# Optimization experiments

Measured on AMD Instinct MI355X. Metric: run time of the kernel, lower is better.

## Reference

```python
import jax, jax.numpy as jnp
import numpy as np


def gcn_conv(x, edge_index, W, b):
    """PyG GCNConv: linear transform, add self-loops, symmetric D^-1/2 A D^-1/2 aggregation, bias."""
    n = x.shape[0]
    h = x @ W  # [N, out] - transform before propagate (small out dim)
    loop = jnp.arange(n, dtype=edge_index.dtype)
    src = jnp.concatenate([edge_index[0], loop])
    dst = jnp.concatenate([edge_index[1], loop])
    deg = jax.ops.segment_sum(jnp.ones_like(dst, dtype=h.dtype), dst, num_segments=n)
    dinv = jnp.where(deg > 0, jax.lax.rsqrt(deg), 0.0)
    norm = dinv[src] * dinv[dst]  # [E+N]
    out = jax.ops.segment_sum(h[src] * norm[:, None], dst, num_segments=n)
    return out + b


def setup_inputs() -> dict:
    key = jax.random.key(0)
    k1, k2, k3, k4, k5, k6 = jax.random.split(key, 6)
    N, F_in, H, C, E = 100000, 128, 16, 2, 3200000
    x = jax.random.normal(k1, (N, F_in), dtype=jnp.float32)
    edge_index = jax.random.randint(k2, (2, E), 0, N, dtype=jnp.int32)
    # Glorot-style init for GCNConv weights
    W1 = jax.random.normal(k3, (F_in, H), dtype=jnp.float32) * (1.0 / np.sqrt(F_in))
    b1 = jnp.zeros((H,), dtype=jnp.float32)
    W2 = jax.random.normal(k4, (H, C), dtype=jnp.float32) * (1.0 / np.sqrt(H))
    b2 = jnp.zeros((C,), dtype=jnp.float32)
    return {"x": x, "edge_index": edge_index, "W1": W1, "b1": b1, "W2": W2, "b2": b2}


def reference(x, edge_index, W1, b1, W2, b2):
    h = gcn_conv(x, edge_index, W1, b1)
    h = jax.nn.relu(h)
    # F.dropout(training=self.training): eval mode -> identity (deterministic reference)
    h = gcn_conv(h, edge_index, W2, b2)
    return jax.nn.log_softmax(h, axis=1)
```

## Files before the change

kernel.cpp:

```cpp
#include <hip/hip_runtime.h>
#include <hip/hip_bf16.h>
#include <math.h>


#define F_IN 128
#define H1 16
#define C_OUT 2
#define SBS 1024
#define LOG_SBS 10
#define NSB_MAX 128
#define SRC_MASK 0x3FFFFF
#define CH1 4096
#define SLICE 128
#define NSLICE (SBS / SLICE)
#define PCAP 5632

typedef int ix4 __attribute__((ext_vector_type(4)));

__device__ __forceinline__ float bflo(unsigned u) { return __uint_as_float(u << 16); }
__device__ __forceinline__ float bfhi(unsigned u) { return __uint_as_float(u & 0xFFFF0000u); }

__global__ __launch_bounds__(256) void k_cnt_gemm1(
    const int* __restrict__ dst0, int* __restrict__ cntm,
    const float* __restrict__ x, const float* __restrict__ W1,
    __hip_bfloat16* __restrict__ h1b,
    int E, int NSB, int nblk, int N) {
    __shared__ int sc[NSB_MAX];
    __shared__ float w[F_IN * H1];
    __shared__ float xt[16 * F_IN];
    int t = threadIdx.x;
    if (blockIdx.x < (unsigned)nblk) {
        if (t < NSB_MAX) sc[t] = 0;
        __syncthreads();
        int e0 = blockIdx.x * CH1, e1 = min(e0 + CH1, E);
        int n4 = (e1 - e0) >> 2;
        const ix4* d4 = (const ix4*)(dst0 + e0);
        for (int i = t; i < n4; i += 256) {
            ix4 d = __builtin_nontemporal_load(&d4[i]);
            atomicAdd(&sc[((unsigned)d.x) >> LOG_SBS], 1);
            atomicAdd(&sc[((unsigned)d.y) >> LOG_SBS], 1);
            atomicAdd(&sc[((unsigned)d.z) >> LOG_SBS], 1);
            atomicAdd(&sc[((unsigned)d.w) >> LOG_SBS], 1);
        }
        for (int e = e0 + n4 * 4 + t; e < e1; e += 256)
            atomicAdd(&sc[((unsigned)dst0[e]) >> LOG_SBS], 1);
        __syncthreads();
        for (int b = t; b < NSB; b += 256)
            cntm[(size_t)b * nblk + blockIdx.x] = sc[b];
    } else {
        int node0 = (blockIdx.x - nblk) * 16;
        const float4* W14 = (const float4*)W1;
        float4* w4 = (float4*)w;
        for (int i = t; i < F_IN * H1 / 4; i += 256) w4[i] = W14[i];
        const float4* x4 = (const float4*)x;
        float4* xt4 = (float4*)xt;
        for (int i = t; i < 16 * F_IN / 4; i += 256) {
            int r = i >> 5;
            int node = node0 + r;
            xt4[i] = (node < N) ? x4[(size_t)node * 32 + (i & 31)]
                                : make_float4(0.f, 0.f, 0.f, 0.f);
        }
        __syncthreads();
        int nsub = t >> 4, f = t & 15;
        int node = node0 + nsub;
        if (node < N) {
            const float* xr = xt + nsub * F_IN;
            float acc = 0.0f;
            #pragma unroll 16
            for (int k = 0; k < F_IN; ++k)
                acc = fmaf(xr[k], w[k * H1 + f], acc);
            h1b[(size_t)node * H1 + f] = __float2bfloat16(acc);
        }
    }
}

__global__ __launch_bounds__(1024) void k_cscan(
    int* __restrict__ cntm, int* __restrict__ tot, int* __restrict__ rp,
    int NSB, int nblk, int E) {
    __shared__ int s[1024];
    int b = blockIdx.x, t = threadIdx.x;
    int* row = cntm + (size_t)b * nblk;
    int own = (t < nblk) ? row[t] : 0;
    s[t] = own;
    __syncthreads();
    for (int off = 1; off < 1024; off <<= 1) {
        int v = (t >= off) ? s[t - off] : 0;
        __syncthreads();
        s[t] += v;
        __syncthreads();
    }
    if (t < nblk) row[t] = s[t] - own;
    if (t == 0) tot[b] = s[1023];
    if (b == 0 && t == 0) rp[NSB * SBS] = E;
}

__global__ __launch_bounds__(256) void k_scat1(
    const int* __restrict__ src0, const int* __restrict__ dst0,
    const int* __restrict__ cntm, unsigned* __restrict__ packed1,
    int E, int NSB, int nblk, int CAP) {
    __shared__ int lcur[NSB_MAX];
    int t = threadIdx.x, blk = blockIdx.x;
    for (int b = t; b < NSB; b += 256)
        lcur[b] = b * CAP + cntm[(size_t)b * nblk + blk];
    __syncthreads();
    int e0 = blk * CH1, e1 = min(e0 + CH1, E);
    int n4 = (e1 - e0) >> 2;
    const ix4* d4 = (const ix4*)(dst0 + e0);
    const ix4* s4 = (const ix4*)(src0 + e0);
    for (int i = t; i < n4; i += 256) {
        ix4 d = __builtin_nontemporal_load(&d4[i]);
        ix4 s = __builtin_nontemporal_load(&s4[i]);
        {
            unsigned dd = (unsigned)d.x;
            int pos = atomicAdd(&lcur[dd >> LOG_SBS], 1);
            packed1[pos] = (unsigned)s.x | ((dd & (SBS - 1)) << 22);
        }
        {
            unsigned dd = (unsigned)d.y;
            int pos = atomicAdd(&lcur[dd >> LOG_SBS], 1);
            packed1[pos] = (unsigned)s.y | ((dd & (SBS - 1)) << 22);
        }
        {
            unsigned dd = (unsigned)d.z;
            int pos = atomicAdd(&lcur[dd >> LOG_SBS], 1);
            packed1[pos] = (unsigned)s.z | ((dd & (SBS - 1)) << 22);
        }
        {
            unsigned dd = (unsigned)d.w;
            int pos = atomicAdd(&lcur[dd >> LOG_SBS], 1);
            packed1[pos] = (unsigned)s.w | ((dd & (SBS - 1)) << 22);
        }
    }
    for (int e = e0 + n4 * 4 + t; e < e1; e += 256) {
        unsigned dd = (unsigned)dst0[e];
        int pos = atomicAdd(&lcur[dd >> LOG_SBS], 1);
        packed1[pos] = (unsigned)src0[e] | ((dd & (SBS - 1)) << 22);
    }
}

__global__ __launch_bounds__(1024) void k_hist(
    const unsigned* __restrict__ packed1, const int* __restrict__ tot,
    int* __restrict__ rp, float* __restrict__ dinv,
    __hip_bfloat16* __restrict__ h1b, int N, int NSB, int CAP) {
    __shared__ int cnt[SBS];
    __shared__ int s2[SBS];
    __shared__ int sbase[NSB_MAX];
    int b = blockIdx.x, t = threadIdx.x;
    if (t < NSB_MAX) sbase[t] = (t < NSB) ? tot[t] : 0;
    cnt[t] = 0;
    __syncthreads();
    if (t == 0) {
        int run = 0;
        #pragma unroll 4
        for (int i = 0; i < NSB_MAX; ++i) { int c = sbase[i]; sbase[i] = run; run += c; }
    }
    __syncthreads();
    int cntb = tot[b];
    int e0 = b * CAP, e1 = e0 + cntb;
    int obase = sbase[b];
    int n4 = cntb >> 2;
    const ix4* p4 = (const ix4*)(packed1 + e0);
    for (int i = t; i < n4; i += 1024) {
        ix4 p = p4[i];
        atomicAdd(&cnt[((unsigned)p.x) >> 22], 1);
        atomicAdd(&cnt[((unsigned)p.y) >> 22], 1);
        atomicAdd(&cnt[((unsigned)p.z) >> 22], 1);
        atomicAdd(&cnt[((unsigned)p.w) >> 22], 1);
    }
    for (int e = e0 + n4 * 4 + t; e < e1; e += 1024)
        atomicAdd(&cnt[packed1[e] >> 22], 1);
    __syncthreads();
    int c = cnt[t];
    s2[t] = c;
    __syncthreads();
    for (int off = 1; off < 1024; off <<= 1) {
        int v = (t >= off) ? s2[t - off] : 0;
        __syncthreads();
        s2[t] += v;
        __syncthreads();
    }
    int ep = s2[t] - c;
    int node = (b << LOG_SBS) + t;
    rp[node] = obase + ep;
    if (node < N) {
        float dv = rsqrtf((float)(c + 1));
        dinv[node] = dv;
        uint4* hrow = (uint4*)(h1b + (size_t)node * H1);
        uint4 s0 = hrow[0], s1 = hrow[1];
        unsigned r0[8];
        float v0, v1;
        #define SCALE_PACK(word, outi) \
            v0 = bflo(word) * dv; v1 = bfhi(word) * dv; \
            r0[outi] = (unsigned)__bfloat16_as_ushort(__float2bfloat16(v0)) | \
                       ((unsigned)__bfloat16_as_ushort(__float2bfloat16(v1)) << 16);
        SCALE_PACK(s0.x, 0) SCALE_PACK(s0.y, 1) SCALE_PACK(s0.z, 2) SCALE_PACK(s0.w, 3)
        SCALE_PACK(s1.x, 4) SCALE_PACK(s1.y, 5) SCALE_PACK(s1.z, 6) SCALE_PACK(s1.w, 7)
        #undef SCALE_PACK
        hrow[0] = make_uint4(r0[0], r0[1], r0[2], r0[3]);
        hrow[1] = make_uint4(r0[4], r0[5], r0[6], r0[7]);
    }
}

__global__ __launch_bounds__(512) void k_place_agg1(
    const unsigned* __restrict__ packed1, const int* __restrict__ tot,
    const int* __restrict__ rp, int* __restrict__ packed2,
    const __hip_bfloat16* __restrict__ h1b, const float* __restrict__ dinv,
    const float* __restrict__ b1, const float* __restrict__ W2,
    float* __restrict__ h2s,
    int N, int NSB, int PADB, int CAP) {
    __shared__ int cur[SLICE];
    __shared__ int lbuf[PCAP];
    int bid = blockIdx.x;
    int s = bid / PADB, b = bid - s * PADB;
    if (b >= NSB) return;
    int t = threadIdx.x;
    int node0 = (b << LOG_SBS) + s * SLICE;
    int g0 = rp[node0];
    if (t < SLICE) cur[t] = rp[node0 + t] - g0;
    int slice_len = rp[node0 + SLICE] - g0;
    __syncthreads();
    int cntb = tot[b];
    int e0 = b * CAP, e1 = e0 + cntb;
    int n4 = cntb >> 2;
    const ix4* p4 = (const ix4*)(packed1 + e0);
    for (int i = t; i < n4; i += 512) {
        ix4 p = p4[i];
        {
            unsigned nd = ((unsigned)p.x) >> 22;
            if ((nd >> 7) == (unsigned)s) {
                int pos = atomicAdd(&cur[nd & (SLICE - 1)], 1);
                if (pos < PCAP) lbuf[pos] = p.x & SRC_MASK;
            }
        }
        {
            unsigned nd = ((unsigned)p.y) >> 22;
            if ((nd >> 7) == (unsigned)s) {
                int pos = atomicAdd(&cur[nd & (SLICE - 1)], 1);
                if (pos < PCAP) lbuf[pos] = p.y & SRC_MASK;
            }
        }
        {
            unsigned nd = ((unsigned)p.z) >> 22;
            if ((nd >> 7) == (unsigned)s) {
                int pos = atomicAdd(&cur[nd & (SLICE - 1)], 1);
                if (pos < PCAP) lbuf[pos] = p.z & SRC_MASK;
            }
        }
        {
            unsigned nd = ((unsigned)p.w) >> 22;
            if ((nd >> 7) == (unsigned)s) {
                int pos = atomicAdd(&cur[nd & (SLICE - 1)], 1);
                if (pos < PCAP) lbuf[pos] = p.w & SRC_MASK;
            }
        }
    }
    for (int e = e0 + n4 * 4 + t; e < e1; e += 512) {
        unsigned p = packed1[e];
        unsigned nd = p >> 22;
        if ((nd >> 7) == (unsigned)s) {
            int pos = atomicAdd(&cur[nd & (SLICE - 1)], 1);
            if (pos < PCAP) lbuf[pos] = (int)(p & SRC_MASK);
        }
    }
    __syncthreads();
    int lim = min(slice_len, PCAP);
    for (int i = t; i < lim; i += 512)
        packed2[g0 + i] = lbuf[i];
    int g = t >> 2, q = t & 3;
    int node = node0 + g;
    if (node < N) {
        const uint2* hv = (const uint2*)h1b;
        float a[4];
        uint2 sv = hv[(size_t)node * 4 + q];
        a[0] = bflo(sv.x); a[1] = bfhi(sv.x); a[2] = bflo(sv.y); a[3] = bfhi(sv.y);
        int lb = rp[node] - g0;
        int le = min(rp[node + 1] - g0, PCAP);
        for (; lb + 8 <= le; lb += 8) {
            int p[8];
            #pragma unroll
            for (int u = 0; u < 8; ++u) p[u] = lbuf[lb + u];
            uint2 v[8];
            #pragma unroll
            for (int u = 0; u < 8; ++u) v[u] = hv[(size_t)p[u] * 4 + q];
            #pragma unroll
            for (int u = 0; u < 8; ++u) {
                a[0] += bflo(v[u].x); a[1] += bfhi(v[u].x);
                a[2] += bflo(v[u].y); a[3] += bfhi(v[u].y);
            }
        }
        for (; lb < le; ++lb) {
            uint2 v = hv[(size_t)lbuf[lb] * 4 + q];
            a[0] += bflo(v.x); a[1] += bfhi(v.x); a[2] += bflo(v.y); a[3] += bfhi(v.y);
        }
        float dv = dinv[node];
        float c0 = 0.f, c1 = 0.f;
        #pragma unroll
        for (int j = 0; j < 4; ++j) {
            int f = q * 4 + j;
            float vv = fmaxf(fmaf(a[j], dv, b1[f]), 0.f);
            c0 = fmaf(vv, W2[f * C_OUT + 0], c0);
            c1 = fmaf(vv, W2[f * C_OUT + 1], c1);
        }
        c0 += __shfl_xor(c0, 1);
        c1 += __shfl_xor(c1, 1);
        c0 += __shfl_xor(c0, 2);
        c1 += __shfl_xor(c1, 2);
        if (q == 0)
            ((float2*)h2s)[node] = make_float2(c0 * dv, c1 * dv);
    }
}

__global__ __launch_bounds__(256) void k_agg2(
    const int* __restrict__ packed2, const int* __restrict__ rp,
    const float* __restrict__ h2s, const float* __restrict__ dinv,
    const float* __restrict__ b2, float* __restrict__ out, int N) {
    int tid = blockIdx.x * 256 + threadIdx.x;
    int n = tid >> 1, q = tid & 1;
    if (n >= N) return;
    float a = h2s[2 * (size_t)n + q];
    int e = rp[n], e1 = rp[n + 1];
    for (; e + 8 <= e1; e += 8) {
        int p[8];
        #pragma unroll
        for (int u = 0; u < 8; ++u) p[u] = packed2[e + u];
        float v[8];
        #pragma unroll
        for (int u = 0; u < 8; ++u) v[u] = h2s[2 * (size_t)p[u] + q];
        #pragma unroll
        for (int u = 0; u < 8; ++u) a += v[u];
    }
    for (; e < e1; ++e) a += h2s[2 * (size_t)packed2[e] + q];
    float dv = dinv[n];
    a = fmaf(a, dv, b2[q]);
    float other = __shfl_xor(a, 1);
    if (q == 0) {
        float a0 = a, a1 = other;
        float m = fmaxf(a0, a1);
        float lse = m + logf(expf(a0 - m) + expf(a1 - m));
        ((float2*)out)[n] = make_float2(a0 - lse, a1 - lse);
    }
}

extern "C" void kernel_launch(void* const* d_in, const int* in_sizes, int n_in,
                              void* d_out, int out_size, void* d_ws, size_t ws_size,
                              hipStream_t stream) {
    const float* x  = (const float*)d_in[0];
    const int* ei   = (const int*)d_in[1];
    const float* W1 = (const float*)d_in[2];
    const float* b1 = (const float*)d_in[3];
    const float* W2 = (const float*)d_in[4];
    const float* b2 = (const float*)d_in[5];
    float* out = (float*)d_out;

    const int N = in_sizes[0] / F_IN;
    const int E = in_sizes[1] / 2;
    const int* src0 = ei;
    const int* dst0 = ei + E;

    const int NSB = (N + SBS - 1) >> LOG_SBS;
    const int nblk = (E + CH1 - 1) / CH1;
    const int PADB = (NSB + 7) & ~7;
    int expSB = (int)(((long long)E << LOG_SBS) / N);
    int CAP = (expSB + expSB / 8 + 2048 + 15) & ~15;

    size_t off = 0;
    float* wsf = (float*)d_ws;
    auto take = [&](size_t nf) { float* p = wsf + off; off += (nf + 3) & ~(size_t)3; return p; };
    float* dinv    = take(N);
    __hip_bfloat16* h1b = (__hip_bfloat16*)take((size_t)N * H1 / 2);
    float* h2s     = take((size_t)N * C_OUT);
    unsigned* packed1 = (unsigned*)take((size_t)NSB * CAP);
    int*   packed2 = (int*)take(E);
    int*   cntm    = (int*)take((size_t)NSB * nblk);
    int*   tot     = (int*)take(NSB_MAX);
    int*   rp      = (int*)take((size_t)NSB * SBS + 1);

    int nbGemm = (N + 15) / 16;
    k_cnt_gemm1<<<nblk + nbGemm, 256, 0, stream>>>(dst0, cntm, x, W1, h1b, E, NSB, nblk, N);
    k_cscan<<<NSB, 1024, 0, stream>>>(cntm, tot, rp, NSB, nblk, E);
    k_scat1<<<nblk, 256, 0, stream>>>(src0, dst0, cntm, packed1, E, NSB, nblk, CAP);
    k_hist<<<NSB, 1024, 0, stream>>>(packed1, tot, rp, dinv, h1b, N, NSB, CAP);
    k_place_agg1<<<NSLICE * PADB, 512, 0, stream>>>(packed1, tot, rp, packed2,
                                                    h1b, dinv, b1, W2, h2s, N, NSB, PADB, CAP);
    k_agg2<<<(2 * N + 255) / 256, 256, 0, stream>>>(packed2, rp, h2s, dinv, b2, out, N);
}
```

Measured before the change: 128.1 us.

## Re-stage slice CSR in LDS for second aggregation instead of writing packed2

Result: no change. 129.6 us (+1.2%).

```diff
diff --git a/kernel.cpp b/kernel.cpp
--- a/kernel.cpp
+++ b/kernel.cpp
@@ -94,20 +94,20 @@
     if (b == 0 && t == 0) rp[NSB * SBS] = E;
 }
 
-__global__ __launch_bounds__(256) void k_scat1(
+__global__ __launch_bounds__(512) void k_scat1(
     const int* __restrict__ src0, const int* __restrict__ dst0,
     const int* __restrict__ cntm, unsigned* __restrict__ packed1,
     int E, int NSB, int nblk, int CAP) {
     __shared__ int lcur[NSB_MAX];
     int t = threadIdx.x, blk = blockIdx.x;
-    for (int b = t; b < NSB; b += 256)
+    for (int b = t; b < NSB; b += 512)
         lcur[b] = b * CAP + cntm[(size_t)b * nblk + blk];
     __syncthreads();
     int e0 = blk * CH1, e1 = min(e0 + CH1, E);
     int n4 = (e1 - e0) >> 2;
     const ix4* d4 = (const ix4*)(dst0 + e0);
     const ix4* s4 = (const ix4*)(src0 + e0);
-    for (int i = t; i < n4; i += 256) {
+    for (int i = t; i < n4; i += 512) {
         ix4 d = __builtin_nontemporal_load(&d4[i]);
         ix4 s = __builtin_nontemporal_load(&s4[i]);
         {
@@ -131,7 +131,7 @@
             packed1[pos] = (unsigned)s.w | ((dd & (SBS - 1)) << 22);
         }
     }
-    for (int e = e0 + n4 * 4 + t; e < e1; e += 256) {
+    for (int e = e0 + n4 * 4 + t; e < e1; e += 512) {
         unsigned dd = (unsigned)dst0[e];
         int pos = atomicAdd(&lcur[dd >> LOG_SBS], 1);
         packed1[pos] = (unsigned)src0[e] | ((dd & (SBS - 1)) << 22);
@@ -201,9 +201,56 @@
     }
 }
 
+__device__ __forceinline__ void stage_slice(
+    const unsigned* __restrict__ packed1, int e0, int cntb,
+    int s, int* cur, int* lbuf, int t, int nthreads) {
+    int n4 = cntb >> 2;
+    const ix4* p4 = (const ix4*)(packed1 + e0);
+    for (int i = t; i < n4; i += nthreads) {
+        ix4 p = p4[i];
+        {
+            unsigned nd = ((unsigned)p.x) >> 22;
+            if ((nd >> 7) == (unsigned)s) {
+                int pos = atomicAdd(&cur[nd & (SLICE - 1)], 1);
+                if (pos < PCAP) lbuf[pos] = p.x & SRC_MASK;
+            }
+        }
+        {
+            unsigned nd = ((unsigned)p.y) >> 22;
+            if ((nd >> 7) == (unsigned)s) {
+                int pos = atomicAdd(&cur[nd & (SLICE - 1)], 1);
+                if (pos < PCAP) lbuf[pos] = p.y & SRC_MASK;
+            }
+        }
+        {
+            unsigned nd = ((unsigned)p.z) >> 22;
+            if ((nd >> 7) == (unsigned)s) {
+                int pos = atomicAdd(&cur[nd & (SLICE - 1)], 1);
+                if (pos < PCAP) lbuf[pos] = p.z & SRC_MASK;
+            }
+        }
+        {
+            unsigned nd = ((unsigned)p.w) >> 22;
+            if ((nd >> 7) == (unsigned)s) {
+                int pos = atomicAdd(&cur[nd & (SLICE - 1)], 1);
+                if (pos < PCAP) lbuf[pos] = p.w & SRC_MASK;
+            }
+        }
+    }
+    int e1 = e0 + cntb;
+    for (int e = e0 + n4 * 4 + t; e < e1; e += nthreads) {
+        unsigned p = packed1[e];
+        unsigned nd = p >> 22;
+        if ((nd >> 7) == (unsigned)s) {
+            int pos = atomicAdd(&cur[nd & (SLICE - 1)], 1);
+            if (pos < PCAP) lbuf[pos] = (int)(p & SRC_MASK);
+        }
+    }
+}
+
 __global__ __launch_bounds__(512) void k_place_agg1(
     const unsigned* __restrict__ packed1, const int* __restrict__ tot,
-    const int* __restrict__ rp, int* __restrict__ packed2,
+    const int* __restrict__ rp,
     const __hip_bfloat16* __restrict__ h1b, const float* __restrict__ dinv,
     const float* __restrict__ b1, const float* __restrict__ W2,
     float* __restrict__ h2s,
@@ -217,55 +264,9 @@
     int node0 = (b << LOG_SBS) + s * SLICE;
     int g0 = rp[node0];
     if (t < SLICE) cur[t] = rp[node0 + t] - g0;
-    int slice_len = rp[node0 + SLICE] - g0;
-    __syncthreads();
-    int cntb = tot[b];
-    int e0 = b * CAP, e1 = e0 + cntb;
-    int n4 = cntb >> 2;
-    const ix4* p4 = (const ix4*)(packed1 + e0);
-    for (int i = t; i < n4; i += 512) {
-        ix4 p = p4[i];
-        {
-            unsigned nd = ((unsigned)p.x) >> 22;
-            if ((nd >> 7) == (unsigned)s) {
-                int pos = atomicAdd(&cur[nd & (SLICE - 1)], 1);
-                if (pos < PCAP) lbuf[pos] = p.x & SRC_MASK;
-            }
-        }
-        {
-            unsigned nd = ((unsigned)p.y) >> 22;
-            if ((nd >> 7) == (unsigned)s) {
-                int pos = atomicAdd(&cur[nd & (SLICE - 1)], 1);
-                if (pos < PCAP) lbuf[pos] = p.y & SRC_MASK;
-            }
-        }
-        {
-            unsigned nd = ((unsigned)p.z) >> 22;
-            if ((nd >> 7) == (unsigned)s) {
-                int pos = atomicAdd(&cur[nd & (SLICE - 1)], 1);
-                if (pos < PCAP) lbuf[pos] = p.z & SRC_MASK;
-            }
-        }
-        {
-            unsigned nd = ((unsigned)p.w) >> 22;
-            if ((nd >> 7) == (unsigned)s) {
-                int pos = atomicAdd(&cur[nd & (SLICE - 1)], 1);
-                if (pos < PCAP) lbuf[pos] = p.w & SRC_MASK;
-            }
-        }
-    }
-    for (int e = e0 + n4 * 4 + t; e < e1; e += 512) {
-        unsigned p = packed1[e];
-        unsigned nd = p >> 22;
-        if ((nd >> 7) == (unsigned)s) {
-            int pos = atomicAdd(&cur[nd & (SLICE - 1)], 1);
-            if (pos < PCAP) lbuf[pos] = (int)(p & SRC_MASK);
-        }
-    }
-    __syncthreads();
-    int lim = min(slice_len, PCAP);
-    for (int i = t; i < lim; i += 512)
-        packed2[g0 + i] = lbuf[i];
+    __syncthreads();
+    stage_slice(packed1, b * CAP, tot[b], s, cur, lbuf, t, 512);
+    __syncthreads();
     int g = t >> 2, q = t & 3;
     int node = node0 + g;
     if (node < N) {
@@ -310,34 +311,52 @@
     }
 }
 
-__global__ __launch_bounds__(256) void k_agg2(
-    const int* __restrict__ packed2, const int* __restrict__ rp,
+__global__ __launch_bounds__(512) void k_place_agg2(
+    const unsigned* __restrict__ packed1, const int* __restrict__ tot,
+    const int* __restrict__ rp,
     const float* __restrict__ h2s, const float* __restrict__ dinv,
-    const float* __restrict__ b2, float* __restrict__ out, int N) {
-    int tid = blockIdx.x * 256 + threadIdx.x;
-    int n = tid >> 1, q = tid & 1;
-    if (n >= N) return;
-    float a = h2s[2 * (size_t)n + q];
-    int e = rp[n], e1 = rp[n + 1];
-    for (; e + 8 <= e1; e += 8) {
-        int p[8];
-        #pragma unroll
-        for (int u = 0; u < 8; ++u) p[u] = packed2[e + u];
-        float v[8];
-        #pragma unroll
-        for (int u = 0; u < 8; ++u) v[u] = h2s[2 * (size_t)p[u] + q];
-        #pragma unroll
-        for (int u = 0; u < 8; ++u) a += v[u];
-    }
-    for (; e < e1; ++e) a += h2s[2 * (size_t)packed2[e] + q];
-    float dv = dinv[n];
-    a = fmaf(a, dv, b2[q]);
-    float other = __shfl_xor(a, 1);
-    if (q == 0) {
-        float a0 = a, a1 = other;
-        float m = fmaxf(a0, a1);
-        float lse = m + logf(expf(a0 - m) + expf(a1 - m));
-        ((float2*)out)[n] = make_float2(a0 - lse, a1 - lse);
+    const float* __restrict__ b2, float* __restrict__ out,
+    int N, int NSB, int PADB, int CAP) {
+    __shared__ int cur[SLICE];
+    __shared__ int lbuf[PCAP];
+    int bid = blockIdx.x;
+    int s = bid / PADB, b = bid - s * PADB;
+    if (b >= NSB) return;
+    int t = threadIdx.x;
+    int node0 = (b << LOG_SBS) + s * SLICE;
+    int g0 = rp[node0];
+    if (t < SLICE) cur[t] = rp[node0 + t] - g0;
+    __syncthreads();
+    stage_slice(packed1, b * CAP, tot[b], s, cur, lbuf, t, 512);
+    __syncthreads();
+    int g = t >> 2, q = t & 3;
+    int ch = q & 1, half = q >> 1;
+    int node = node0 + g;
+    if (node < N) {
+        float a = half ? 0.f : h2s[2 * (size_t)node + ch];
+        int lb = rp[node] - g0 + half;
+        int le = min(rp[node + 1] - g0, PCAP);
+        for (; lb + 16 <= le; lb += 16) {
+            int p[8];
+            #pragma unroll
+            for (int u = 0; u < 8; ++u) p[u] = lbuf[lb + 2 * u];
+            float v[8];
+            #pragma unroll
+            for (int u = 0; u < 8; ++u) v[u] = h2s[2 * (size_t)p[u] + ch];
+            #pragma unroll
+            for (int u = 0; u < 8; ++u) a += v[u];
+        }
+        for (; lb < le; lb += 2) a += h2s[2 * (size_t)lbuf[lb] + ch];
+        a += __shfl_xor(a, 2);
+        float dv = dinv[node];
+        a = fmaf(a, dv, b2[ch]);
+        float other = __shfl_xor(a, 1);
+        if (q == 0) {
+            float a0 = a, a1 = other;
+            float m = fmaxf(a0, a1);
+            float lse = m + logf(expf(a0 - m) + expf(a1 - m));
+            ((float2*)out)[node] = make_float2(a0 - lse, a1 - lse);
+        }
     }
 }
 
@@ -370,7 +389,6 @@
     __hip_bfloat16* h1b = (__hip_bfloat16*)take((size_t)N * H1 / 2);
     float* h2s     = take((size_t)N * C_OUT);
     unsigned* packed1 = (unsigned*)take((size_t)NSB * CAP);
-    int*   packed2 = (int*)take(E);
     int*   cntm    = (int*)take((size_t)NSB * nblk);
     int*   tot     = (int*)take(NSB_MAX);
     int*   rp      = (int*)take((size_t)NSB * SBS + 1);
@@ -378,9 +396,10 @@
     int nbGemm = (N + 15) / 16;
     k_cnt_gemm1<<<nblk + nbGemm, 256, 0, stream>>>(dst0, cntm, x, W1, h1b, E, NSB, nblk, N);
     k_cscan<<<NSB, 1024, 0, stream>>>(cntm, tot, rp, NSB, nblk, E);
-    k_scat1<<<nblk, 256, 0, stream>>>(src0, dst0, cntm, packed1, E, NSB, nblk, CAP);
+    k_scat1<<<nblk, 512, 0, stream>>>(src0, dst0, cntm, packed1, E, NSB, nblk, CAP);
     k_hist<<<NSB, 1024, 0, stream>>>(packed1, tot, rp, dinv, h1b, N, NSB, CAP);
-    k_place_agg1<<<NSLICE * PADB, 512, 0, stream>>>(packed1, tot, rp, packed2,
+    k_place_agg1<<<NSLICE * PADB, 512, 0, stream>>>(packed1, tot, rp,
                                                     h1b, dinv, b1, W2, h2s, N, NSB, PADB, CAP);
-    k_agg2<<<(2 * N + 255) / 256, 256, 0, stream>>>(packed2, rp, h2s, dinv, b2, out, N);
-}
+    k_place_agg2<<<NSLICE * PADB, 512, 0, stream>>>(packed1, tot, rp,
+                                                    h2s, dinv, b2, out, N, NSB, PADB, CAP);
+}
```
